# Optimization experiments

Hardware: AMD Instinct MI355X
Metric: run time of the kernel (lower is better)

## Reference

```python
import jax, jax.numpy as jnp
import numpy as np

WS = 7        # window_size
SHIFT = 3     # shift_size
HEADS = 6
DIM = 192
HIDDEN = DIM * 6  # mlp_ratio=6
EPS = 1e-5


def _rel_pos_index(ws):
    # static relative-position index, (ws*ws, ws*ws) int
    coords = np.stack(np.meshgrid(np.arange(ws), np.arange(ws), indexing='ij')).reshape(2, -1)
    rel = coords[:, :, None] - coords[:, None, :]            # (2, N, N)
    rel = rel.transpose(1, 2, 0)                             # (N, N, 2)
    rel[:, :, 0] += ws - 1
    rel[:, :, 1] += ws - 1
    rel[:, :, 0] *= 2 * ws - 1
    return rel.sum(-1)


def _layernorm(t, g, b):
    m = t.mean(-1, keepdims=True)
    v = jnp.mean((t - m) ** 2, axis=-1, keepdims=True)
    return (t - m) * jax.lax.rsqrt(v + EPS) * g + b


def setup_inputs() -> dict:
    key = jax.random.key(0)
    ks = jax.random.split(key, 8)
    B, H, W = 16, 56, 56
    x = jax.random.normal(ks[0], (B, H * W, DIM), dtype=jnp.float32)
    p = lambda k, s: (jax.random.normal(k, s, dtype=jnp.float32) * 0.02)
    return {
        'x': x, 'H': H, 'W': W,
        'ln1_g': jnp.ones((DIM,), jnp.float32), 'ln1_b': jnp.zeros((DIM,), jnp.float32),
        'qkv_w': p(ks[1], (3 * DIM, DIM)), 'qkv_b': jnp.zeros((3 * DIM,), jnp.float32),
        'rpb': p(ks[2], ((2 * WS - 1) ** 2, HEADS)),
        'proj_w': p(ks[3], (DIM, DIM)), 'proj_b': jnp.zeros((DIM,), jnp.float32),
        'ln2_g': jnp.ones((DIM,), jnp.float32), 'ln2_b': jnp.zeros((DIM,), jnp.float32),
        'fc1_w': p(ks[4], (HIDDEN, DIM)), 'fc1_b': jnp.zeros((HIDDEN,), jnp.float32),
        'fc2_w': p(ks[5], (DIM, HIDDEN)), 'fc2_b': jnp.zeros((DIM,), jnp.float32),
    }


def reference(x, H, W, ln1_g, ln1_b, qkv_w, qkv_b, rpb, proj_w, proj_b,
              ln2_g, ln2_b, fc1_w, fc1_b, fc2_w, fc2_b):
    B, L, C = x.shape
    hd = C // HEADS
    shortcut = x
    h = _layernorm(x, ln1_g, ln1_b).reshape(B, H, W, C)
    pad_r = (WS - W % WS) % WS
    pad_b = (WS - H % WS) % WS
    h = jnp.pad(h, ((0, 0), (0, pad_b), (0, pad_r), (0, 0)))
    Hp, Wp = H + pad_b, W + pad_r
    if SHIFT > 0:
        h = jnp.roll(h, (-SHIFT, -SHIFT), axis=(1, 2))
    # window partition -> (nW*B, WS*WS, C)
    h = h.reshape(B, Hp // WS, WS, Wp // WS, WS, C).transpose(0, 1, 3, 2, 4, 5)
    h = h.reshape(-1, WS * WS, C)
    nB, N, _ = h.shape
    qkv = (h @ qkv_w.T + qkv_b).reshape(nB, N, 3, HEADS, hd).transpose(2, 0, 3, 1, 4)
    q, k, v = qkv[0], qkv[1], qkv[2]       # (nB, heads, N, hd)
    scale = hd ** -0.5
    attn = jnp.einsum('bhnd,bhmd->bhnm', q * scale, k)
    idx = _rel_pos_index(WS)
    bias = rpb[idx.reshape(-1)].reshape(N, N, HEADS).transpose(2, 0, 1)  # (heads, N, N)
    attn = jax.nn.softmax(attn + bias[None], axis=-1)
    out = jnp.einsum('bhnm,bhmd->bhnd', attn, v).transpose(0, 2, 1, 3).reshape(nB, N, C)
    out = out @ proj_w.T + proj_b
    # window reverse -> (B, Hp, Wp, C)
    out = out.reshape(B, Hp // WS, Wp // WS, WS, WS, C).transpose(0, 1, 3, 2, 4, 5)
    out = out.reshape(B, Hp, Wp, C)
    if SHIFT > 0:
        out = jnp.roll(out, (SHIFT, SHIFT), axis=(1, 2))
    out = out[:, :H, :W, :].reshape(B, H * W, C)
    x = shortcut + out
    h2 = _layernorm(x, ln2_g, ln2_b)
    h2 = jax.nn.gelu(h2 @ fc1_w.T + fc1_b, approximate=False)
    return x + (h2 @ fc2_w.T + fc2_b)
```

## Files before the change

kernel.cpp:

```cpp
#include <hip/hip_runtime.h>

typedef unsigned short u16;
typedef __bf16 bf16x8 __attribute__((ext_vector_type(8)));
typedef __bf16 bf16x2_t __attribute__((ext_vector_type(2)));
typedef float f32x4 __attribute__((ext_vector_type(4)));

#define AS1 __attribute__((address_space(1)))
#define AS3 __attribute__((address_space(3)))

__device__ __forceinline__ void gld16(const void* g, void* l) {
  __builtin_amdgcn_global_load_lds((const AS1 void*)g, (AS3 void*)l, 16, 0, 0);
}

__device__ __forceinline__ u16 f2bf(float f) {
  union { float f; unsigned int u; } v; v.f = f;
  unsigned int u = v.u;
  u += 0x7fffu + ((u >> 16) & 1u);
  return (u16)(u >> 16);
}
__device__ __forceinline__ float bf2f(u16 h) {
  union { unsigned int u; float f; } v; v.u = ((unsigned int)h) << 16; return v.f;
}
__device__ __forceinline__ unsigned int pk2(float a, float b) {
#if __has_builtin(__builtin_amdgcn_cvt_pk_bf16_f32)
  union { bf16x2_t v; unsigned int u; } c;
  c.v = __builtin_amdgcn_cvt_pk_bf16_f32(a, b);
  return c.u;
#else
  return (unsigned int)f2bf(a) | ((unsigned int)f2bf(b) << 16);
#endif
}
__device__ __forceinline__ float gelu_f(float v) {
  float u = v * (1.5957691216f + 0.0713548163f * v * v);
  return v * __builtin_amdgcn_rcpf(1.0f + __expf(-u));
}

__global__ __launch_bounds__(256) void cast_weights(
    const float* __restrict__ w0, const float* __restrict__ w1,
    const float* __restrict__ w2, const float* __restrict__ w3,
    u16* __restrict__ o0, u16* __restrict__ o1,
    u16* __restrict__ o2, u16* __restrict__ o3) {
  int i = blockIdx.x * 256 + threadIdx.x;
  if (i < 110592) o0[i] = f2bf(w0[i]);
  if (i < 36864) {
    int n = i / 192, kp = i - n * 192;
    int h = kp >> 5, dp = kp & 31;
    int d = (dp & 1) ? ((dp >> 1) + 16) : (dp >> 1);
    o1[i] = f2bf(w1[n * 192 + h * 32 + d]);
  }
  if (i < 221184) o2[i] = f2bf(w2[i]);
  if (i < 221184) o3[i] = f2bf(w3[i]);
}

__global__ __launch_bounds__(256) void build_btab(
    const float* __restrict__ rpb, float* __restrict__ btab) {
  int id = blockIdx.x * 256 + threadIdx.x;
  int head = id >> 12;
  int m = (id >> 6) & 63;
  int r = id & 63;
  float v;
  if (m >= 49) v = -1e30f;
  else if (r >= 49) v = 0.0f;
  else {
    int mi = m / 7, mj = m - mi * 7;
    int ri = r / 7, rj = r - ri * 7;
    v = rpb[((ri - mi + 6) * 13 + (rj - mj + 6)) * 6 + head];
  }
  btab[id] = v;
}

__global__ __launch_bounds__(256) void ln_kernel(
    const float* __restrict__ x, const float* __restrict__ g,
    const float* __restrict__ b, u16* __restrict__ out) {
  int row = blockIdx.x * 4 + (threadIdx.x >> 6);
  int lane = threadIdx.x & 63;
  const float* xr = x + (long)row * 192;
  float e0 = xr[lane], e1 = xr[lane + 64], e2 = xr[lane + 128];
  float s = e0 + e1 + e2;
  #pragma unroll
  for (int o = 1; o < 64; o <<= 1) s += __shfl_xor(s, o);
  float mean = s * (1.0f / 192.0f);
  float d0 = e0 - mean, d1 = e1 - mean, d2 = e2 - mean;
  float q = d0 * d0 + d1 * d1 + d2 * d2;
  #pragma unroll
  for (int o = 1; o < 64; o <<= 1) q += __shfl_xor(q, o);
  float rstd = rsqrtf(q * (1.0f / 192.0f) + 1e-5f);
  u16* orow = out + (long)row * 192;
  orow[lane]       = f2bf(d0 * rstd * g[lane]       + b[lane]);
  orow[lane + 64]  = f2bf(d1 * rstd * g[lane + 64]  + b[lane + 64]);
  orow[lane + 128] = f2bf(d2 * rstd * g[lane + 128] + b[lane + 128]);
}

template<int MODE>
__global__ __launch_bounds__(256, 3) void gemm_kernel(
    const u16* __restrict__ A, const u16* __restrict__ W,
    const float* __restrict__ bias, const float* __restrict__ resid,
    void* __restrict__ out, int N, int K) {
  constexpr int TT = 20;
  constexpr int BUF = TT * 512;
  __shared__ u16 lds[2 * BUF];
  float* ct = (float*)lds;
  const int tid = threadIdx.x;
  const int wave = tid >> 6, lane = tid & 63;
  const int wm = wave >> 1, wn = wave & 1;
  const int quad = lane >> 4, l15 = lane & 15;
  const long bm = (long)blockIdx.x * 128;
  const int bn = blockIdx.y * 192;
  const int NC = K >> 5;

  for (int t = wave; t < TT; t += 4) {
    const u16* g = (t < 8)
        ? (A + (bm + t * 16 + l15) * (long)K + quad * 8)
        : (W + (long)(bn + (t - 8) * 16 + l15) * K + quad * 8);
    gld16(g, &lds[t * 512]);
  }
  __syncthreads();

  f32x4 acc[4][6] = {};
  for (int c = 0; c < NC; c++) {
    const int cur = c & 1;
    if (c + 1 < NC) {
      const int kof = (c + 1) * 32 + quad * 8;
      u16* nb = &lds[(cur ^ 1) * BUF];
      for (int t = wave; t < TT; t += 4) {
        const u16* g = (t < 8)
            ? (A + (bm + t * 16 + l15) * (long)K + kof)
            : (W + (long)(bn + (t - 8) * 16 + l15) * K + kof);
        gld16(g, nb + t * 512);
      }
    }
    const u16* buf = lds + cur * BUF;
    bf16x8 af[4];
    #pragma unroll
    for (int mt = 0; mt < 4; mt++)
      af[mt] = *(const bf16x8*)&buf[(wm * 4 + mt) * 512 + lane * 8];
    #pragma unroll
    for (int nt = 0; nt < 6; nt++) {
      bf16x8 bfr = *(const bf16x8*)&buf[(8 + wn * 6 + nt) * 512 + lane * 8];
      #pragma unroll
      for (int mt = 0; mt < 4; mt++)
        acc[mt][nt] = __builtin_amdgcn_mfma_f32_16x16x32_bf16(af[mt], bfr, acc[mt][nt], 0, 0, 0);
    }
    __syncthreads();
  }

  #pragma unroll
  for (int h = 0; h < 2; h++) {
    #pragma unroll
    for (int g = 0; g < 2; g++) {
      if (wm == h && wn == g) {
        #pragma unroll
        for (int nt = 0; nt < 6; nt++) {
          int col = nt * 16 + l15;
          float bi = bias[bn + g * 96 + col];
          #pragma unroll
          for (int mt = 0; mt < 4; mt++) {
            int row0 = mt * 16 + quad * 4;
            #pragma unroll
            for (int j = 0; j < 4; j++)
              ct[(row0 + j) * 100 + col] = acc[mt][nt][j] + bi;
          }
        }
      }
      __syncthreads();
      #pragma unroll
      for (int it = 0; it < 6; it++) {
        int cc = it * 256 + tid;
        int row = cc / 24, i = cc - row * 24;
        float4 v = *(const float4*)&ct[row * 100 + i * 4];
        long idx = (bm + h * 64 + row) * (long)N + bn + g * 96 + i * 4;
        if (MODE == 2) {
          const float4 rv = *(const float4*)(resid + idx);
          v.x += rv.x; v.y += rv.y; v.z += rv.z; v.w += rv.w;
          *(float4*)((float*)out + idx) = v;
        } else {
          if (MODE == 1) {
            v.x = gelu_f(v.x); v.y = gelu_f(v.y); v.z = gelu_f(v.z); v.w = gelu_f(v.w);
          }
          uint2 pk;
          pk.x = pk2(v.x, v.y);
          pk.y = pk2(v.z, v.w);
          *(uint2*)((u16*)out + idx) = pk;
        }
      }
      if (!(h == 1 && g == 1)) __syncthreads();
    }
  }
}

__global__ __launch_bounds__(256) void attn_kernel(
    const u16* __restrict__ qkv, const float* __restrict__ btab,
    u16* __restrict__ attn) {
  __shared__ u16 lds[4 * 7040];
  __shared__ float sbias[64 * 65];
  int tid = threadIdx.x;
  int wave = tid >> 6, lane = tid & 63;
  int quad = lane >> 4, l15 = lane & 15;
  int head = blockIdx.x % 6;
  int grp = blockIdx.x / 6;
  int win = grp * 4 + wave;
  int b = win >> 6, wy = (win >> 3) & 7, wx = win & 7;
  u16* lp = lds + wave * 7040;
  u16* lvt = lp + 4608;
  float* rsum = (float*)(lp + 6912);

  {
    const float* bsrc = btab + head * 4096;
    #pragma unroll
    for (int i = 0; i < 4; i++) {
      int idx4 = tid + i * 256;
      float4 v = *(const float4*)(bsrc + idx4 * 4);
      float* dst = &sbias[(idx4 >> 4) * 65 + (idx4 & 15) * 4];
      dst[0] = v.x; dst[1] = v.y; dst[2] = v.z; dst[3] = v.w;
    }
  }

  bf16x8 qb[4], ka[4];
  #pragma unroll
  for (int t = 0; t < 4; t++) {
    int n = t * 16 + l15;
    uint4 qv = {0, 0, 0, 0}, kv = {0, 0, 0, 0}, vv = {0, 0, 0, 0};
    if (n < 49) {
      int i = n / 7, j = n - i * 7;
      int y = wy * 7 + i + 3;  if (y >= 56) y -= 56;
      int xx = wx * 7 + j + 3; if (xx >= 56) xx -= 56;
      long base = ((long)(b * 3136 + y * 56 + xx)) * 576 + head * 32 + quad * 8;
      qv = *(const uint4*)(qkv + base);
      kv = *(const uint4*)(qkv + base + 192);
      vv = *(const uint4*)(qkv + base + 384);
    }
    qb[t] = *(const bf16x8*)&qv;
    ka[t] = *(const bf16x8*)&kv;
    const u16* vp = (const u16*)&vv;
    #pragma unroll
    for (int d = 0; d < 8; d++) lvt[(quad * 8 + d) * 72 + n] = vp[d];
  }

  f32x4 s[4][4];
  const f32x4 fz = {0.0f, 0.0f, 0.0f, 0.0f};
  #pragma unroll
  for (int tm = 0; tm < 4; tm++)
    #pragma unroll
    for (int tr = 0; tr < 4; tr++)
      s[tm][tr] = __builtin_amdgcn_mfma_f32_16x16x32_bf16(ka[tm], qb[tr], fz, 0, 0, 0);

  __syncthreads();

  const float scale = 0.17677669529663687f;
  float mx[4] = {-1e30f, -1e30f, -1e30f, -1e30f};
  #pragma unroll
  for (int tm = 0; tm < 4; tm++) {
    int m0 = tm * 16 + quad * 4;
    #pragma unroll
    for (int tr = 0; tr < 4; tr++) {
      int r = tr * 16 + l15;
      #pragma unroll
      for (int j = 0; j < 4; j++) {
        float v = s[tm][tr][j] * scale + sbias[(m0 + j) * 65 + r];
        s[tm][tr][j] = v;
        mx[tr] = fmaxf(mx[tr], v);
      }
    }
  }
  #pragma unroll
  for (int tr = 0; tr < 4; tr++) {
    mx[tr] = fmaxf(mx[tr], __shfl_xor(mx[tr], 16));
    mx[tr] = fmaxf(mx[tr], __shfl_xor(mx[tr], 32));
  }
  float sm[4] = {0.f, 0.f, 0.f, 0.f};
  #pragma unroll
  for (int tm = 0; tm < 4; tm++) {
    #pragma unroll
    for (int tr = 0; tr < 4; tr++) {
      int r = tr * 16 + l15;
      float e0 = __expf(s[tm][tr][0] - mx[tr]);
      float e1 = __expf(s[tm][tr][1] - mx[tr]);
      float e2 = __expf(s[tm][tr][2] - mx[tr]);
      float e3 = __expf(s[tm][tr][3] - mx[tr]);
      sm[tr] += (e0 + e1) + (e2 + e3);
      uint2 pk;
      pk.x = pk2(e0, e1);
      pk.y = pk2(e2, e3);
      *(uint2*)&lp[r * 72 + tm * 16 + quad * 4] = pk;
    }
  }
  #pragma unroll
  for (int tr = 0; tr < 4; tr++) {
    sm[tr] += __shfl_xor(sm[tr], 16);
    sm[tr] += __shfl_xor(sm[tr], 32);
  }
  if (quad == 0) {
    #pragma unroll
    for (int tr = 0; tr < 4; tr++) rsum[tr * 16 + l15] = __builtin_amdgcn_rcpf(sm[tr]);
  }

  f32x4 o[4][2] = {};
  #pragma unroll
  for (int ks = 0; ks < 2; ks++) {
    bf16x8 vb0 = *(const bf16x8*)&lvt[(l15) * 72 + ks * 32 + quad * 8];
    bf16x8 vb1 = *(const bf16x8*)&lvt[(16 + l15) * 72 + ks * 32 + quad * 8];
    #pragma unroll
    for (int rt = 0; rt < 4; rt++) {
      bf16x8 pf = *(const bf16x8*)&lp[(rt * 16 + l15) * 72 + ks * 32 + quad * 8];
      o[rt][0] = __builtin_amdgcn_mfma_f32_16x16x32_bf16(pf, vb0, o[rt][0], 0, 0, 0);
      o[rt][1] = __builtin_amdgcn_mfma_f32_16x16x32_bf16(pf, vb1, o[rt][1], 0, 0, 0);
    }
  }
  #pragma unroll
  for (int rt = 0; rt < 4; rt++) {
    #pragma unroll
    for (int j = 0; j < 4; j++) {
      int r = rt * 16 + quad * 4 + j;
      if (r < 49) {
        float inv = rsum[r];
        int i = r / 7, jj = r - i * 7;
        int y = wy * 7 + i + 3;   if (y >= 56) y -= 56;
        int xx = wx * 7 + jj + 3; if (xx >= 56) xx -= 56;
        long base = ((long)(b * 3136 + y * 56 + xx)) * 192 + head * 32 + 2 * l15;
        *(unsigned int*)&attn[base] = pk2(o[rt][0][j] * inv, o[rt][1][j] * inv);
      }
    }
  }
}

extern "C" void kernel_launch(void* const* d_in, const int* in_sizes, int n_in,
                              void* d_out, int out_size, void* d_ws, size_t ws_size,
                              hipStream_t stream) {
  (void)in_sizes; (void)n_in; (void)out_size; (void)ws_size;
  const float* x      = (const float*)d_in[0];
  const float* ln1_g  = (const float*)d_in[3];
  const float* ln1_b  = (const float*)d_in[4];
  const float* qkv_w  = (const float*)d_in[5];
  const float* qkv_b  = (const float*)d_in[6];
  const float* rpb    = (const float*)d_in[7];
  const float* proj_w = (const float*)d_in[8];
  const float* proj_b = (const float*)d_in[9];
  const float* ln2_g  = (const float*)d_in[10];
  const float* ln2_b  = (const float*)d_in[11];
  const float* fc1_w  = (const float*)d_in[12];
  const float* fc1_b  = (const float*)d_in[13];
  const float* fc2_w  = (const float*)d_in[14];
  const float* fc2_b  = (const float*)d_in[15];

  char* ws = (char*)d_ws;
  float* x2   = (float*)(ws + 0);
  u16* hA     = (u16*)(ws + 38535168);
  float* btab = (float*)(ws + 38535168);
  u16* qkv    = (u16*)(ws + 57802752);
  u16* attn   = (u16*)(ws + 115605504);
  u16* hid    = (u16*)(ws + 57802752);
  u16* wbuf   = (u16*)(ws + 173408256);
  u16* qkv_wb  = wbuf;
  u16* proj_wb = wbuf + 110592;
  u16* fc1_wb  = wbuf + 147456;
  u16* fc2_wb  = wbuf + 368640;

  cast_weights<<<dim3(864), 256, 0, stream>>>(qkv_w, proj_w, fc1_w, fc2_w,
                                              qkv_wb, proj_wb, fc1_wb, fc2_wb);
  ln_kernel<<<dim3(12544), 256, 0, stream>>>(x, ln1_g, ln1_b, hA);
  gemm_kernel<0><<<dim3(392, 3), 256, 0, stream>>>(hA, qkv_wb, qkv_b, nullptr,
                                                   qkv, 576, 192);
  build_btab<<<dim3(96), 256, 0, stream>>>(rpb, btab);
  attn_kernel<<<dim3(1536), 256, 0, stream>>>(qkv, btab, attn);
  gemm_kernel<2><<<dim3(392, 1), 256, 0, stream>>>(attn, proj_wb, proj_b, x,
                                                   x2, 192, 192);
  ln_kernel<<<dim3(12544), 256, 0, stream>>>(x2, ln2_g, ln2_b, hA);
  gemm_kernel<1><<<dim3(392, 6), 256, 0, stream>>>(hA, fc1_wb, fc1_b, nullptr,
                                                   hid, 1152, 192);
  gemm_kernel<2><<<dim3(392, 1), 256, 0, stream>>>(hid, fc2_wb, fc2_b, x2,
                                                   (float*)d_out, 192, 1152);
}
```

Measured before the change: 340.7 us.

## Fuse LayerNorm2 into proj GEMM epilogue and simplify GEMM tile staging

A new GEMM mode computes the proj output plus bias plus residual, writes x2, and then applies LayerNorm2 in the epilogue, emitting the bf16 normalized activations directly. This removes the separate LN kernel launch and its re-read of x2. The global-to-LDS staging now uses precomputed per-wave pointers that advance each k-step instead of recomputing addresses in a loop. Launch bounds rise to 4 blocks per CU for the non-fused modes. LN2 now uses a single-pass E[x²]-mean² variance, which is slightly less numerically robust, and the fused mode needs a larger LDS buffer.

```diff
diff --git a/kernel.cpp b/kernel.cpp
--- a/kernel.cpp
+++ b/kernel.cpp
@@ -92,13 +92,16 @@
 }
 
 template<int MODE>
-__global__ __launch_bounds__(256, 3) void gemm_kernel(
+__global__ __launch_bounds__(256, (MODE == 3) ? 3 : 4) void gemm_kernel(
     const u16* __restrict__ A, const u16* __restrict__ W,
     const float* __restrict__ bias, const float* __restrict__ resid,
-    void* __restrict__ out, int N, int K) {
+    void* __restrict__ out, u16* __restrict__ out2,
+    const float* __restrict__ g2, const float* __restrict__ b2,
+    int N, int K) {
   constexpr int TT = 20;
   constexpr int BUF = TT * 512;
-  __shared__ u16 lds[2 * BUF];
+  constexpr int LDSU = (MODE == 3) ? 25600 : (2 * BUF);
+  __shared__ u16 lds[LDSU];
   float* ct = (float*)lds;
   const int tid = threadIdx.x;
   const int wave = tid >> 6, lane = tid & 63;
@@ -108,27 +111,30 @@
   const int bn = blockIdx.y * 192;
   const int NC = K >> 5;
 
-  for (int t = wave; t < TT; t += 4) {
-    const u16* g = (t < 8)
-        ? (A + (bm + t * 16 + l15) * (long)K + quad * 8)
-        : (W + (long)(bn + (t - 8) * 16 + l15) * K + quad * 8);
-    gld16(g, &lds[t * 512]);
-  }
+  const u16* pA0 = A + (bm + wave * 16 + l15) * (long)K + quad * 8;
+  const u16* pA1 = pA0 + 64 * (long)K;
+  const u16* pB0 = W + (long)(bn + wave * 16 + l15) * K + quad * 8;
+  const u16* pB1 = pB0 + 64 * (long)K;
+  const u16* pB2 = pB0 + 128 * (long)K;
+  const int d0 = wave * 512, d1 = (wave + 4) * 512, d2 = (wave + 8) * 512,
+            d3 = (wave + 12) * 512, d4 = (wave + 16) * 512;
+
+  auto stage5 = [&](u16* dst) {
+    gld16(pA0, dst + d0);
+    gld16(pA1, dst + d1);
+    gld16(pB0, dst + d2);
+    gld16(pB1, dst + d3);
+    gld16(pB2, dst + d4);
+    pA0 += 32; pA1 += 32; pB0 += 32; pB1 += 32; pB2 += 32;
+  };
+
+  stage5(lds);
   __syncthreads();
 
   f32x4 acc[4][6] = {};
   for (int c = 0; c < NC; c++) {
     const int cur = c & 1;
-    if (c + 1 < NC) {
-      const int kof = (c + 1) * 32 + quad * 8;
-      u16* nb = &lds[(cur ^ 1) * BUF];
-      for (int t = wave; t < TT; t += 4) {
-        const u16* g = (t < 8)
-            ? (A + (bm + t * 16 + l15) * (long)K + kof)
-            : (W + (long)(bn + (t - 8) * 16 + l15) * K + kof);
-        gld16(g, nb + t * 512);
-      }
-    }
+    if (c + 1 < NC) stage5(&lds[(cur ^ 1) * BUF]);
     const u16* buf = lds + cur * BUF;
     bf16x8 af[4];
     #pragma unroll
@@ -142,6 +148,59 @@
         acc[mt][nt] = __builtin_amdgcn_mfma_f32_16x16x32_bf16(af[mt], bfr, acc[mt][nt], 0, 0, 0);
     }
     __syncthreads();
+  }
+
+  if (MODE == 3) {
+    const int r = tid >> 2, seg = tid & 3;
+    #pragma unroll
+    for (int h = 0; h < 2; h++) {
+      if (wm == h) {
+        #pragma unroll
+        for (int nt = 0; nt < 6; nt++) {
+          int col = wn * 96 + nt * 16 + l15;
+          float bi = bias[col];
+          #pragma unroll
+          for (int mt = 0; mt < 4; mt++) {
+            int row0 = mt * 16 + quad * 4;
+            #pragma unroll
+            for (int j = 0; j < 4; j++)
+              ct[(row0 + j) * 200 + col] = acc[mt][nt][j] + bi;
+          }
+        }
+      }
+      __syncthreads();
+      long grow = (bm + h * 64 + r) * 192 + seg * 48;
+      float sum = 0.f, sq = 0.f;
+      #pragma unroll
+      for (int k = 0; k < 12; k++) {
+        float4 v = *(const float4*)&ct[r * 200 + seg * 48 + k * 4];
+        const float4 rv = *(const float4*)(resid + grow + k * 4);
+        v.x += rv.x; v.y += rv.y; v.z += rv.z; v.w += rv.w;
+        *(float4*)&ct[r * 200 + seg * 48 + k * 4] = v;
+        *(float4*)((float*)out + grow + k * 4) = v;
+        sum += (v.x + v.y) + (v.z + v.w);
+        sq += (v.x * v.x + v.y * v.y) + (v.z * v.z + v.w * v.w);
+      }
+      sum += __shfl_xor(sum, 1); sum += __shfl_xor(sum, 2);
+      sq  += __shfl_xor(sq, 1);  sq  += __shfl_xor(sq, 2);
+      float mean = sum * (1.0f / 192.0f);
+      float var = fmaxf(sq * (1.0f / 192.0f) - mean * mean, 0.0f);
+      float rstd = rsqrtf(var + 1e-5f);
+      #pragma unroll
+      for (int k = 0; k < 12; k++) {
+        float4 v = *(const float4*)&ct[r * 200 + seg * 48 + k * 4];
+        const float4 gv = *(const float4*)(g2 + seg * 48 + k * 4);
+        const float4 bv = *(const float4*)(b2 + seg * 48 + k * 4);
+        uint2 pk;
+        pk.x = pk2((v.x - mean) * rstd * gv.x + bv.x,
+                   (v.y - mean) * rstd * gv.y + bv.y);
+        pk.y = pk2((v.z - mean) * rstd * gv.z + bv.z,
+                   (v.w - mean) * rstd * gv.w + bv.w);
+        *(uint2*)(out2 + grow + k * 4) = pk;
+      }
+      if (h == 0) __syncthreads();
+    }
+    return;
   }
 
   #pragma unroll
@@ -359,14 +418,17 @@
                                               qkv_wb, proj_wb, fc1_wb, fc2_wb);
   ln_kernel<<<dim3(12544), 256, 0, stream>>>(x, ln1_g, ln1_b, hA);
   gemm_kernel<0><<<dim3(392, 3), 256, 0, stream>>>(hA, qkv_wb, qkv_b, nullptr,
-                                                   qkv, 576, 192);
+                                                   qkv, nullptr, nullptr, nullptr,
+                                                   576, 192);
   build_btab<<<dim3(96), 256, 0, stream>>>(rpb, btab);
   attn_kernel<<<dim3(1536), 256, 0, stream>>>(qkv, btab, attn);
-  gemm_kernel<2><<<dim3(392, 1), 256, 0, stream>>>(attn, proj_wb, proj_b, x,
-                                                   x2, 192, 192);
-  ln_kernel<<<dim3(12544), 256, 0, stream>>>(x2, ln2_g, ln2_b, hA);
+  gemm_kernel<3><<<dim3(392, 1), 256, 0, stream>>>(attn, proj_wb, proj_b, x,
+                                                   x2, hA, ln2_g, ln2_b,
+                                                   192, 192);
   gemm_kernel<1><<<dim3(392, 6), 256, 0, stream>>>(hA, fc1_wb, fc1_b, nullptr,
-                                                   hid, 1152, 192);
+                                                   hid, nullptr, nullptr, nullptr,
+                                                   1152, 192);
   gemm_kernel<2><<<dim3(392, 1), 256, 0, stream>>>(hid, fc2_wb, fc2_b, x2,
-                                                   (float*)d_out, 192, 1152);
-}
+                                                   (float*)d_out, nullptr, nullptr, nullptr,
+                                                   192, 1152);
+}
```

After: 430.1 us. 26.3% more time.

## Fuse fc1+GELU+fc2 MLP into one kernel keeping hidden activations in LDS

Applied to the files above, without the earlier changes.

Replaces the separate fc1 (with GELU) and fc2 GEMM launches with a single mlp_kernel. Each block handles 64 rows and loops over six 192-wide hidden chunks. For each chunk it computes fc1+GELU into LDS, then immediately accumulates fc2 from it, double-buffering weight tiles via global_load_lds. This removes the round trip of the large bf16 hidden tensor through global memory. The cost is more LDS per block and fewer rows per block (64), and the whole fc1 weight matrix is re-read from cache by every block.

```diff
diff --git a/kernel.cpp b/kernel.cpp
--- a/kernel.cpp
+++ b/kernel.cpp
@@ -174,9 +174,6 @@
           v.x += rv.x; v.y += rv.y; v.z += rv.z; v.w += rv.w;
           *(float4*)((float*)out + idx) = v;
         } else {
-          if (MODE == 1) {
-            v.x = gelu_f(v.x); v.y = gelu_f(v.y); v.z = gelu_f(v.z); v.w = gelu_f(v.w);
-          }
           uint2 pk;
           pk.x = pk2(v.x, v.y);
           pk.y = pk2(v.z, v.w);
@@ -185,6 +182,134 @@
       }
       if (!(h == 1 && g == 1)) __syncthreads();
     }
+  }
+}
+
+__global__ __launch_bounds__(256, 2) void mlp_kernel(
+    const u16* __restrict__ hA, const u16* __restrict__ W1,
+    const float* __restrict__ b1, const u16* __restrict__ W2,
+    const float* __restrict__ b2, const float* __restrict__ resid,
+    float* __restrict__ out) {
+  __shared__ u16 wbuf[2 * 6144];
+  __shared__ u16 hid[12800];
+  __shared__ float sb1[1152];
+  float* ct = (float*)hid;
+  const int tid = threadIdx.x;
+  const int wave = tid >> 6, lane = tid & 63;
+  const int wm = wave >> 1, wn = wave & 1;
+  const int quad = lane >> 4, l15 = lane & 15;
+  const long bm = (long)blockIdx.x * 64;
+
+  const long w1b = (long)(wave * 16 + l15) * 192 + quad * 8;
+  const long w2b = (long)(wave * 16 + l15) * 1152 + quad * 8;
+  const int dt0 = wave * 512, dt1 = (wave + 4) * 512, dt2 = (wave + 8) * 512;
+
+  auto stageW1 = [&](int hc, int kc, int pb) {
+    const u16* g = W1 + w1b + hc * 36864 + kc * 32;
+    u16* d = wbuf + pb * 6144;
+    gld16(g, d + dt0);
+    gld16(g + 12288, d + dt1);
+    gld16(g + 24576, d + dt2);
+  };
+  auto stageW2 = [&](int hc, int kc, int pb) {
+    const u16* g = W2 + w2b + hc * 192 + kc * 32;
+    u16* d = wbuf + pb * 6144;
+    gld16(g, d + dt0);
+    gld16(g + 73728, d + dt1);
+    gld16(g + 147456, d + dt2);
+  };
+
+  stageW1(0, 0, 0);
+  #pragma unroll
+  for (int it = 0; it < 2; ++it) {
+    int idx = it * 256 + tid;
+    if (idx < 288) *(float4*)&sb1[idx * 4] = *(const float4*)&b1[idx * 4];
+  }
+  bf16x8 haf[2][6];
+  #pragma unroll
+  for (int mt = 0; mt < 2; mt++)
+    #pragma unroll
+    for (int kc = 0; kc < 6; kc++)
+      haf[mt][kc] = *(const bf16x8*)&hA[(bm + wm * 32 + mt * 16 + l15) * 192 + kc * 32 + quad * 8];
+  __syncthreads();
+
+  f32x4 acc2[2][6] = {};
+  for (int hc = 0; hc < 6; ++hc) {
+    f32x4 acc1[6][2];
+    #pragma unroll
+    for (int nt = 0; nt < 6; nt++) {
+      f32x4 bv = *(const f32x4*)&sb1[hc * 192 + wn * 96 + nt * 16 + quad * 4];
+      acc1[nt][0] = bv;
+      acc1[nt][1] = bv;
+    }
+    #pragma unroll
+    for (int kc = 0; kc < 6; kc++) {
+      if (kc < 5) stageW1(hc, kc + 1, (kc & 1) ^ 1);
+      else        stageW2(hc, 0, (kc & 1) ^ 1);
+      const u16* buf = wbuf + (kc & 1) * 6144;
+      #pragma unroll
+      for (int nt = 0; nt < 6; nt++) {
+        bf16x8 wf = *(const bf16x8*)&buf[(wn * 6 + nt) * 512 + lane * 8];
+        acc1[nt][0] = __builtin_amdgcn_mfma_f32_16x16x32_bf16(wf, haf[0][kc], acc1[nt][0], 0, 0, 0);
+        acc1[nt][1] = __builtin_amdgcn_mfma_f32_16x16x32_bf16(wf, haf[1][kc], acc1[nt][1], 0, 0, 0);
+      }
+      __syncthreads();
+    }
+    #pragma unroll
+    for (int nt = 0; nt < 6; nt++)
+      #pragma unroll
+      for (int mt = 0; mt < 2; mt++) {
+        uint2 pk;
+        pk.x = pk2(gelu_f(acc1[nt][mt][0]), gelu_f(acc1[nt][mt][1]));
+        pk.y = pk2(gelu_f(acc1[nt][mt][2]), gelu_f(acc1[nt][mt][3]));
+        *(uint2*)&hid[(wm * 32 + mt * 16 + l15) * 200 + wn * 96 + nt * 16 + quad * 4] = pk;
+      }
+    __syncthreads();
+    #pragma unroll
+    for (int kc = 0; kc < 6; kc++) {
+      if (kc < 5)      stageW2(hc, kc + 1, (kc & 1) ^ 1);
+      else if (hc < 5) stageW1(hc + 1, 0, (kc & 1) ^ 1);
+      const u16* buf = wbuf + (kc & 1) * 6144;
+      bf16x8 hf0 = *(const bf16x8*)&hid[(wm * 32 + l15) * 200 + kc * 32 + quad * 8];
+      bf16x8 hf1 = *(const bf16x8*)&hid[(wm * 32 + 16 + l15) * 200 + kc * 32 + quad * 8];
+      #pragma unroll
+      for (int nt = 0; nt < 6; nt++) {
+        bf16x8 wf = *(const bf16x8*)&buf[(wn * 6 + nt) * 512 + lane * 8];
+        acc2[0][nt] = __builtin_amdgcn_mfma_f32_16x16x32_bf16(hf0, wf, acc2[0][nt], 0, 0, 0);
+        acc2[1][nt] = __builtin_amdgcn_mfma_f32_16x16x32_bf16(hf1, wf, acc2[1][nt], 0, 0, 0);
+      }
+      __syncthreads();
+    }
+  }
+
+  #pragma unroll
+  for (int g = 0; g < 2; g++) {
+    if (wn == g) {
+      #pragma unroll
+      for (int nt = 0; nt < 6; nt++) {
+        int col = nt * 16 + l15;
+        float bi = b2[g * 96 + col];
+        #pragma unroll
+        for (int mt = 0; mt < 2; mt++) {
+          int row0 = wm * 32 + mt * 16 + quad * 4;
+          #pragma unroll
+          for (int j = 0; j < 4; j++)
+            ct[(row0 + j) * 100 + col] = acc2[mt][nt][j] + bi;
+        }
+      }
+    }
+    __syncthreads();
+    #pragma unroll
+    for (int it = 0; it < 6; it++) {
+      int cc = it * 256 + tid;
+      int row = cc / 24, i = cc - row * 24;
+      float4 v = *(const float4*)&ct[row * 100 + i * 4];
+      long idx = (bm + row) * 192 + g * 96 + i * 4;
+      const float4 rv = *(const float4*)(resid + idx);
+      v.x += rv.x; v.y += rv.y; v.z += rv.z; v.w += rv.w;
+      *(float4*)(out + idx) = v;
+    }
+    if (g == 0) __syncthreads();
   }
 }
 
@@ -348,7 +473,6 @@
   float* btab = (float*)(ws + 38535168);
   u16* qkv    = (u16*)(ws + 57802752);
   u16* attn   = (u16*)(ws + 115605504);
-  u16* hid    = (u16*)(ws + 57802752);
   u16* wbuf   = (u16*)(ws + 173408256);
   u16* qkv_wb  = wbuf;
   u16* proj_wb = wbuf + 110592;
@@ -365,8 +489,6 @@
   gemm_kernel<2><<<dim3(392, 1), 256, 0, stream>>>(attn, proj_wb, proj_b, x,
                                                    x2, 192, 192);
   ln_kernel<<<dim3(12544), 256, 0, stream>>>(x2, ln2_g, ln2_b, hA);
-  gemm_kernel<1><<<dim3(392, 6), 256, 0, stream>>>(hA, fc1_wb, fc1_b, nullptr,
-                                                   hid, 1152, 192);
-  gemm_kernel<2><<<dim3(392, 1), 256, 0, stream>>>(hid, fc2_wb, fc2_b, x2,
-                                                   (float*)d_out, 192, 1152);
-}
+  mlp_kernel<<<dim3(784), 256, 0, stream>>>(hA, fc1_wb, fc1_b, fc2_wb, fc2_b,
+                                            x2, (float*)d_out);
+}
```

Result: no change. 342.4 us (+0.5%).

## Add register-resident-A GEMM for K=192 layers and simplify staging pointers

Applied to the files above, without the earlier changes.

Adds a GEMM kernel for K=192 that loads each wave's whole A panel into registers and stages the full weight tile for a 96-wide N slice into LDS once. This removes the K-loop double buffering and the LDS-transpose epilogue. It is used for the qkv, proj and fc1 projections with twice as many N blocks. The existing GEMM gets precomputed staging pointers and a simpler epilogue index computation. The direct epilogue uses scalar strided stores, which may coalesce poorly, and rereads A across more N blocks.

```diff
diff --git a/kernel.cpp b/kernel.cpp
--- a/kernel.cpp
+++ b/kernel.cpp
@@ -89,6 +89,71 @@
   orow[lane]       = f2bf(d0 * rstd * g[lane]       + b[lane]);
   orow[lane + 64]  = f2bf(d1 * rstd * g[lane + 64]  + b[lane + 64]);
   orow[lane + 128] = f2bf(d2 * rstd * g[lane + 128] + b[lane + 128]);
+}
+
+template<int MODE>
+__global__ __launch_bounds__(256, 3) void wsgemm_kernel(
+    const u16* __restrict__ A, const u16* __restrict__ W,
+    const float* __restrict__ bias, const float* __restrict__ resid,
+    void* __restrict__ out, int N) {
+  __shared__ u16 wlds[36 * 512];
+  const int tid = threadIdx.x;
+  const int wave = tid >> 6, lane = tid & 63;
+  const int quad = lane >> 4, l15 = lane & 15;
+  const int bn = blockIdx.y * 96;
+  const long bm = (long)blockIdx.x * 128 + wave * 32;
+
+  bf16x8 af[2][6];
+  #pragma unroll
+  for (int mt = 0; mt < 2; mt++)
+    #pragma unroll
+    for (int kc = 0; kc < 6; kc++)
+      af[mt][kc] = *(const bf16x8*)&A[(bm + mt * 16 + l15) * 192 + kc * 32 + quad * 8];
+
+  #pragma unroll
+  for (int i = 0; i < 9; i++) {
+    int t = wave + i * 4;
+    int kc = t / 6, nt = t - kc * 6;
+    gld16(W + (long)(bn + nt * 16 + l15) * 192 + kc * 32 + quad * 8,
+          &wlds[t * 512]);
+  }
+
+  float bi[6];
+  #pragma unroll
+  for (int nt = 0; nt < 6; nt++) bi[nt] = bias[bn + nt * 16 + l15];
+
+  __syncthreads();
+
+  f32x4 acc[2][6] = {};
+  #pragma unroll
+  for (int kc = 0; kc < 6; kc++) {
+    #pragma unroll
+    for (int nt = 0; nt < 6; nt++) {
+      bf16x8 wf = *(const bf16x8*)&wlds[(kc * 6 + nt) * 512 + lane * 8];
+      acc[0][nt] = __builtin_amdgcn_mfma_f32_16x16x32_bf16(af[0][kc], wf, acc[0][nt], 0, 0, 0);
+      acc[1][nt] = __builtin_amdgcn_mfma_f32_16x16x32_bf16(af[1][kc], wf, acc[1][nt], 0, 0, 0);
+    }
+  }
+
+  #pragma unroll
+  for (int mt = 0; mt < 2; mt++) {
+    #pragma unroll
+    for (int nt = 0; nt < 6; nt++) {
+      const long col = bn + nt * 16 + l15;
+      #pragma unroll
+      for (int j = 0; j < 4; j++) {
+        const long row = bm + mt * 16 + quad * 4 + j;
+        const long idx = row * (long)N + col;
+        float v = acc[mt][nt][j] + bi[nt];
+        if (MODE == 2) {
+          ((float*)out)[idx] = v + resid[idx];
+        } else {
+          if (MODE == 1) v = gelu_f(v);
+          ((u16*)out)[idx] = f2bf(v);
+        }
+      }
+    }
+  }
 }
 
 template<int MODE>
@@ -108,27 +173,27 @@
   const int bn = blockIdx.y * 192;
   const int NC = K >> 5;
 
-  for (int t = wave; t < TT; t += 4) {
-    const u16* g = (t < 8)
-        ? (A + (bm + t * 16 + l15) * (long)K + quad * 8)
-        : (W + (long)(bn + (t - 8) * 16 + l15) * K + quad * 8);
-    gld16(g, &lds[t * 512]);
-  }
+  const u16* sp[5];
+  int sd[5];
+  #pragma unroll
+  for (int i = 0; i < 5; i++) {
+    int t = wave + i * 4;
+    sp[i] = (t < 8) ? (A + (bm + t * 16 + l15) * (long)K + quad * 8)
+                    : (W + (long)(bn + (t - 8) * 16 + l15) * K + quad * 8);
+    sd[i] = t * 512;
+  }
+  auto stage = [&](u16* dst) {
+    #pragma unroll
+    for (int i = 0; i < 5; i++) { gld16(sp[i], dst + sd[i]); sp[i] += 32; }
+  };
+
+  stage(lds);
   __syncthreads();
 
   f32x4 acc[4][6] = {};
   for (int c = 0; c < NC; c++) {
     const int cur = c & 1;
-    if (c + 1 < NC) {
-      const int kof = (c + 1) * 32 + quad * 8;
-      u16* nb = &lds[(cur ^ 1) * BUF];
-      for (int t = wave; t < TT; t += 4) {
-        const u16* g = (t < 8)
-            ? (A + (bm + t * 16 + l15) * (long)K + kof)
-            : (W + (long)(bn + (t - 8) * 16 + l15) * K + kof);
-        gld16(g, nb + t * 512);
-      }
-    }
+    if (c + 1 < NC) stage(&lds[(cur ^ 1) * BUF]);
     const u16* buf = lds + cur * BUF;
     bf16x8 af[4];
     #pragma unroll
@@ -144,6 +209,7 @@
     __syncthreads();
   }
 
+  const int frow = tid >> 2, seg = tid & 3;
   #pragma unroll
   for (int h = 0; h < 2; h++) {
     #pragma unroll
@@ -163,12 +229,12 @@
         }
       }
       __syncthreads();
+      const float* cp = &ct[frow * 100 + seg * 4];
+      long gbase = (bm + h * 64 + frow) * (long)N + bn + g * 96 + seg * 4;
       #pragma unroll
-      for (int it = 0; it < 6; it++) {
-        int cc = it * 256 + tid;
-        int row = cc / 24, i = cc - row * 24;
-        float4 v = *(const float4*)&ct[row * 100 + i * 4];
-        long idx = (bm + h * 64 + row) * (long)N + bn + g * 96 + i * 4;
+      for (int k = 0; k < 6; k++) {
+        float4 v = *(const float4*)(cp + k * 16);
+        long idx = gbase + k * 16;
         if (MODE == 2) {
           const float4 rv = *(const float4*)(resid + idx);
           v.x += rv.x; v.y += rv.y; v.z += rv.z; v.w += rv.w;
@@ -358,15 +424,15 @@
   cast_weights<<<dim3(864), 256, 0, stream>>>(qkv_w, proj_w, fc1_w, fc2_w,
                                               qkv_wb, proj_wb, fc1_wb, fc2_wb);
   ln_kernel<<<dim3(12544), 256, 0, stream>>>(x, ln1_g, ln1_b, hA);
-  gemm_kernel<0><<<dim3(392, 3), 256, 0, stream>>>(hA, qkv_wb, qkv_b, nullptr,
-                                                   qkv, 576, 192);
+  wsgemm_kernel<0><<<dim3(392, 6), 256, 0, stream>>>(hA, qkv_wb, qkv_b, nullptr,
+                                                     qkv, 576);
   build_btab<<<dim3(96), 256, 0, stream>>>(rpb, btab);
   attn_kernel<<<dim3(1536), 256, 0, stream>>>(qkv, btab, attn);
-  gemm_kernel<2><<<dim3(392, 1), 256, 0, stream>>>(attn, proj_wb, proj_b, x,
-                                                   x2, 192, 192);
+  wsgemm_kernel<2><<<dim3(392, 2), 256, 0, stream>>>(attn, proj_wb, proj_b, x,
+                                                     x2, 192);
   ln_kernel<<<dim3(12544), 256, 0, stream>>>(x2, ln2_g, ln2_b, hA);
-  gemm_kernel<1><<<dim3(392, 6), 256, 0, stream>>>(hA, fc1_wb, fc1_b, nullptr,
-                                                   hid, 1152, 192);
+  wsgemm_kernel<1><<<dim3(392, 12), 256, 0, stream>>>(hA, fc1_wb, fc1_b, nullptr,
+                                                      hid, 1152);
   gemm_kernel<2><<<dim3(392, 1), 256, 0, stream>>>(hid, fc2_wb, fc2_b, x2,
                                                    (float*)d_out, 192, 1152);
 }
```

New measurement: 324.3 us. 4.8% less time.
